# Optimization experiments

Hardware: AMD Instinct MI355X
Metric: run time of the kernel (lower is better)

Reference implementation:

```python
import jax, jax.numpy as jnp
import numpy as np

# Module constants (from init_kwargs)
X_RANGE = (-10.0, 10.0)
Y_RANGE = (-10.0, 10.0)
N_X = 64
N_Y = 64
B = 16
N_CTX = 1024


def make_grid():
    # x counted forward, y counted backwards (image-row convention):
    # grid[k*N_X + j] = (xs[j], ys[k]) with ys from max to min.
    xs = jnp.linspace(X_RANGE[0], X_RANGE[1], N_X, dtype=jnp.float32)
    ys = jnp.linspace(Y_RANGE[1], Y_RANGE[0], N_Y, dtype=jnp.float32)
    gx, gy = jnp.meshgrid(xs, ys)          # each (N_Y, N_X)
    return jnp.stack([gx, gy], axis=-1).reshape(-1, 2)  # (G, 2)


def setup_inputs() -> dict:
    key = jax.random.key(0)
    k1, k2 = jax.random.split(key)
    X = jax.random.uniform(k1, (B, N_CTX, 2), dtype=jnp.float32,
                           minval=X_RANGE[0], maxval=X_RANGE[1])
    Y = jax.random.normal(k2, (B, N_CTX, 2), dtype=jnp.float32)
    log_l_scale = jnp.zeros((), dtype=jnp.float32)  # log(1.0)
    return {"X": X, "Y": Y, "log_l_scale": log_l_scale}


def reference(X, Y, log_l_scale):
    grid = make_grid()                                  # (G, 2)
    l = jnp.exp(log_l_scale)
    # squared distances via expansion to avoid a (B,G,n,2) intermediate
    g2 = jnp.sum(grid * grid, axis=-1)                  # (G,)
    x2 = jnp.sum(X * X, axis=-1)                        # (B, n)
    gx = jnp.einsum('gd,bnd->bgn', grid, X)             # (B, G, n)
    d2 = g2[None, :, None] + x2[:, None, :] - 2.0 * gx  # (B, G, n)
    Gram = jnp.exp(-0.5 * d2 / (l * l))                 # RBF kernel, B=1
    # expand Y with a leading ones (density) channel
    ones = jnp.ones(Y.shape[:2] + (1,), dtype=Y.dtype)
    EY = jnp.concatenate([ones, Y], axis=-1)            # (B, n, 3)
    FM = jnp.einsum('bgn,bnc->bgc', Gram, EY)           # (B, G, 3)
    dens = FM[..., 0:1]
    FM = jnp.concatenate([dens, FM[..., 1:] / dens], axis=-1)
    # (B, G, 3) -> (B, 3, N_Y, N_X)
    return FM.reshape(X.shape[0], N_Y, N_X, 3).transpose(0, 3, 1, 2)
```

## Files before the change

kernel.cpp:

```cpp
#include <hip/hip_runtime.h>
#include <hip/hip_bf16.h>
#include <math.h>


#define NB     16
#define NCTX   1024
#define NG     4096
#define NSPLIT 16
#define NC     64

__global__ __launch_bounds__(256, 1)
void ee_partial(const float* __restrict__ X,
                const float* __restrict__ Y,
                const float* __restrict__ log_l_scale,
                float* __restrict__ ws) {
    const int b  = blockIdx.x >> 4;
    const int nc = blockIdx.x & 15;
    const int n0 = nc * NC;

    const float step  = 20.0f / 63.0f;
    const float scale = -0.72134752044448170f * expf(-2.0f * log_l_scale[0]);

    __shared__ float  wx[NC][64];
    __shared__ float  wy[NC][64];
    __shared__ float2 sy[NC];

    const float2* Xb = (const float2*)(X + (size_t)b * NCTX * 2);
    const float2* Yb = (const float2*)(Y + (size_t)b * NCTX * 2);

    for (int idx = threadIdx.x; idx < NC * 64; idx += 256) {
        const int j = idx >> 6, i = idx & 63;
        const float2 xv = Xb[n0 + j];
        const float dx = (-10.0f + step * (float)i) - xv.x;
        const float dy = ( 10.0f - step * (float)i) - xv.y;
        wx[j][i] = exp2f(dx * dx * scale);
        wy[j][i] = exp2f(dy * dy * scale);
    }
    if (threadIdx.x < NC) sy[threadIdx.x] = Yb[n0 + threadIdx.x];
    __syncthreads();

    const int tx = threadIdx.x & 15;
    const int ty = threadIdx.x >> 4;
    const int ix0 = tx * 4;
    const int iy0 = ty * 4;

    float4 ad[4] = {{0,0,0,0},{0,0,0,0},{0,0,0,0},{0,0,0,0}};
    float4 a1[4] = {{0,0,0,0},{0,0,0,0},{0,0,0,0},{0,0,0,0}};
    float4 a2[4] = {{0,0,0,0},{0,0,0,0},{0,0,0,0},{0,0,0,0}};

#pragma unroll 4
    for (int n = 0; n < NC; ++n) {
        const float4 wxv = *(const float4*)&wx[n][ix0];
        const float4 wyv = *(const float4*)&wy[n][iy0];
        const float2 yv  = sy[n];
        const float wys[4] = {wyv.x, wyv.y, wyv.z, wyv.w};
#pragma unroll
        for (int s = 0; s < 4; ++s) {
            const float w  = wys[s];
            const float q1 = w * yv.x;
            const float q2 = w * yv.y;
            ad[s].x = fmaf(wxv.x, w, ad[s].x);  ad[s].y = fmaf(wxv.y, w, ad[s].y);
            ad[s].z = fmaf(wxv.z, w, ad[s].z);  ad[s].w = fmaf(wxv.w, w, ad[s].w);
            a1[s].x = fmaf(wxv.x, q1, a1[s].x); a1[s].y = fmaf(wxv.y, q1, a1[s].y);
            a1[s].z = fmaf(wxv.z, q1, a1[s].z); a1[s].w = fmaf(wxv.w, q1, a1[s].w);
            a2[s].x = fmaf(wxv.x, q2, a2[s].x); a2[s].y = fmaf(wxv.y, q2, a2[s].y);
            a2[s].z = fmaf(wxv.z, q2, a2[s].z); a2[s].w = fmaf(wxv.w, q2, a2[s].w);
        }
    }

    float* base = ws + ((size_t)(b * NSPLIT + nc)) * 3 * NG;
#pragma unroll
    for (int s = 0; s < 4; ++s) {
        const int g = (iy0 + s) * 64 + ix0;
        *(float4*)&base[g]          = ad[s];
        *(float4*)&base[NG + g]     = a1[s];
        *(float4*)&base[2*NG + g]   = a2[s];
    }
}

__global__ __launch_bounds__(256)
void ee_reduce(const float* __restrict__ ws, float* __restrict__ out) {
    const int t = blockIdx.x * 256 + threadIdx.x;
    const int b = t >> 12, g = t & 4095;
    const float* base = ws + (size_t)b * NSPLIT * 3 * NG;
    float a0 = 0, a1 = 0, a2 = 0;
#pragma unroll
    for (int nc = 0; nc < NSPLIT; ++nc) {
        const float* p = base + nc * 3 * NG;
        a0 += p[g];
        a1 += p[NG + g];
        a2 += p[2 * NG + g];
    }
    const float inv = 1.0f / a0;
    float* ob = out + (size_t)b * 3 * NG;
    ob[g]          = a0;
    ob[NG + g]     = a1 * inv;
    ob[2 * NG + g] = a2 * inv;
}

extern "C" void kernel_launch(void* const* d_in, const int* in_sizes, int n_in,
                              void* d_out, int out_size, void* d_ws, size_t ws_size,
                              hipStream_t stream) {
    const float* X    = (const float*)d_in[0];
    const float* Y    = (const float*)d_in[1];
    const float* logl = (const float*)d_in[2];
    float* out = (float*)d_out;
    float* ws  = (float*)d_ws;

    ee_partial<<<dim3(NB * NSPLIT), dim3(256), 0, stream>>>(X, Y, logl, ws);
    ee_reduce <<<dim3(NB * NG / 256), dim3(256), 0, stream>>>(ws, out);
}
```

Before: 72.62 us.

## Fuse partial and reduce kernels by tiling grid instead of splitting context

```diff
diff --git a/kernel.cpp b/kernel.cpp
--- a/kernel.cpp
+++ b/kernel.cpp
@@ -1,101 +1,91 @@
 #include <hip/hip_runtime.h>
-#include <hip/hip_bf16.h>
 #include <math.h>
 
 
 #define NB     16
 #define NCTX   1024
 #define NG     4096
-#define NSPLIT 16
-#define NC     64
+#define NSTAGE 128
+#define NCHUNK (NCTX / NSTAGE)
+#define ROWLEN (NSTAGE + 4)
 
 __global__ __launch_bounds__(256, 1)
-void ee_partial(const float* __restrict__ X,
-                const float* __restrict__ Y,
-                const float* __restrict__ log_l_scale,
-                float* __restrict__ ws) {
-    const int b  = blockIdx.x >> 4;
-    const int nc = blockIdx.x & 15;
-    const int n0 = nc * NC;
+void ee_fused(const float* __restrict__ X,
+              const float* __restrict__ Y,
+              const float* __restrict__ log_l_scale,
+              float* __restrict__ out) {
+    const int b    = blockIdx.x >> 4;
+    const int tile = blockIdx.x & 15;
+    const int ix0  = (tile & 3) * 16;
+    const int iy0  = (tile >> 2) * 16;
 
     const float step  = 20.0f / 63.0f;
     const float scale = -0.72134752044448170f * expf(-2.0f * log_l_scale[0]);
 
-    __shared__ float  wx[NC][64];
-    __shared__ float  wy[NC][64];
-    __shared__ float2 sy[NC];
+    __shared__ float wxs[2][16][ROWLEN];
+    __shared__ float wys[2][16][ROWLEN];
+    __shared__ float y0s[2][NSTAGE];
+    __shared__ float y1s[2][NSTAGE];
 
     const float2* Xb = (const float2*)(X + (size_t)b * NCTX * 2);
     const float2* Yb = (const float2*)(Y + (size_t)b * NCTX * 2);
 
-    for (int idx = threadIdx.x; idx < NC * 64; idx += 256) {
-        const int j = idx >> 6, i = idx & 63;
-        const float2 xv = Xb[n0 + j];
-        const float dx = (-10.0f + step * (float)i) - xv.x;
-        const float dy = ( 10.0f - step * (float)i) - xv.y;
-        wx[j][i] = exp2f(dx * dx * scale);
-        wy[j][i] = exp2f(dy * dy * scale);
-    }
-    if (threadIdx.x < NC) sy[threadIdx.x] = Yb[n0 + threadIdx.x];
+    const int t   = threadIdx.x;
+    const int ixl = t & 15;
+    const int iyl = t >> 4;
+
+    auto build = [&](int c, int p) {
+        const int n0 = c * NSTAGE;
+        const int n  = t & (NSTAGE - 1);
+        const int ih = t >> 7;
+        const float2 xv = Xb[n0 + n];
+        const float bx = -10.0f + step * (float)ix0 - xv.x;
+        const float by =  10.0f - step * (float)iy0 - xv.y;
+#pragma unroll
+        for (int e = 0; e < 8; ++e) {
+            const int i = 2 * e + ih;
+            const float dx = bx + step * (float)i;
+            const float dy = by - step * (float)i;
+            wxs[p][i][n] = exp2f(dx * dx * scale);
+            wys[p][i][n] = exp2f(dy * dy * scale);
+        }
+        if (t < NSTAGE) {
+            const float2 yv = Yb[n0 + t];
+            y0s[p][t] = yv.x;
+            y1s[p][t] = yv.y;
+        }
+    };
+
+    float dens = 0.0f, s1 = 0.0f, s2 = 0.0f;
+
+    build(0, 0);
     __syncthreads();
 
-    const int tx = threadIdx.x & 15;
-    const int ty = threadIdx.x >> 4;
-    const int ix0 = tx * 4;
-    const int iy0 = ty * 4;
-
-    float4 ad[4] = {{0,0,0,0},{0,0,0,0},{0,0,0,0},{0,0,0,0}};
-    float4 a1[4] = {{0,0,0,0},{0,0,0,0},{0,0,0,0},{0,0,0,0}};
-    float4 a2[4] = {{0,0,0,0},{0,0,0,0},{0,0,0,0},{0,0,0,0}};
+    for (int c = 0; c < NCHUNK; ++c) {
+        const int p = c & 1;
+        if (c + 1 < NCHUNK) build(c + 1, p ^ 1);
 
 #pragma unroll 4
-    for (int n = 0; n < NC; ++n) {
-        const float4 wxv = *(const float4*)&wx[n][ix0];
-        const float4 wyv = *(const float4*)&wy[n][iy0];
-        const float2 yv  = sy[n];
-        const float wys[4] = {wyv.x, wyv.y, wyv.z, wyv.w};
-#pragma unroll
-        for (int s = 0; s < 4; ++s) {
-            const float w  = wys[s];
-            const float q1 = w * yv.x;
-            const float q2 = w * yv.y;
-            ad[s].x = fmaf(wxv.x, w, ad[s].x);  ad[s].y = fmaf(wxv.y, w, ad[s].y);
-            ad[s].z = fmaf(wxv.z, w, ad[s].z);  ad[s].w = fmaf(wxv.w, w, ad[s].w);
-            a1[s].x = fmaf(wxv.x, q1, a1[s].x); a1[s].y = fmaf(wxv.y, q1, a1[s].y);
-            a1[s].z = fmaf(wxv.z, q1, a1[s].z); a1[s].w = fmaf(wxv.w, q1, a1[s].w);
-            a2[s].x = fmaf(wxv.x, q2, a2[s].x); a2[s].y = fmaf(wxv.y, q2, a2[s].y);
-            a2[s].z = fmaf(wxv.z, q2, a2[s].z); a2[s].w = fmaf(wxv.w, q2, a2[s].w);
+        for (int n4 = 0; n4 < NSTAGE; n4 += 4) {
+            const float4 wx4 = *(const float4*)&wxs[p][ixl][n4];
+            const float4 wy4 = *(const float4*)&wys[p][iyl][n4];
+            const float4 ya  = *(const float4*)&y0s[p][n4];
+            const float4 yb  = *(const float4*)&y1s[p][n4];
+            float w;
+            w = wx4.x * wy4.x; dens += w; s1 = fmaf(w, ya.x, s1); s2 = fmaf(w, yb.x, s2);
+            w = wx4.y * wy4.y; dens += w; s1 = fmaf(w, ya.y, s1); s2 = fmaf(w, yb.y, s2);
+            w = wx4.z * wy4.z; dens += w; s1 = fmaf(w, ya.z, s1); s2 = fmaf(w, yb.z, s2);
+            w = wx4.w * wy4.w; dens += w; s1 = fmaf(w, ya.w, s1); s2 = fmaf(w, yb.w, s2);
         }
+        __syncthreads();
     }
 
-    float* base = ws + ((size_t)(b * NSPLIT + nc)) * 3 * NG;
-#pragma unroll
-    for (int s = 0; s < 4; ++s) {
-        const int g = (iy0 + s) * 64 + ix0;
-        *(float4*)&base[g]          = ad[s];
-        *(float4*)&base[NG + g]     = a1[s];
-        *(float4*)&base[2*NG + g]   = a2[s];
-    }
-}
-
-__global__ __launch_bounds__(256)
-void ee_reduce(const float* __restrict__ ws, float* __restrict__ out) {
-    const int t = blockIdx.x * 256 + threadIdx.x;
-    const int b = t >> 12, g = t & 4095;
-    const float* base = ws + (size_t)b * NSPLIT * 3 * NG;
-    float a0 = 0, a1 = 0, a2 = 0;
-#pragma unroll
-    for (int nc = 0; nc < NSPLIT; ++nc) {
-        const float* p = base + nc * 3 * NG;
-        a0 += p[g];
-        a1 += p[NG + g];
-        a2 += p[2 * NG + g];
-    }
-    const float inv = 1.0f / a0;
+    const int g = (iy0 + iyl) * 64 + (ix0 + ixl);
     float* ob = out + (size_t)b * 3 * NG;
-    ob[g]          = a0;
-    ob[NG + g]     = a1 * inv;
-    ob[2 * NG + g] = a2 * inv;
+    const float inv = 1.0f / dens;
+    ob[g]          = dens;
+    ob[NG + g]     = s1 * inv;
+    ob[2 * NG + g] = s2 * inv;
 }
 
 extern "C" void kernel_launch(void* const* d_in, const int* in_sizes, int n_in,
@@ -105,8 +95,7 @@
     const float* Y    = (const float*)d_in[1];
     const float* logl = (const float*)d_in[2];
     float* out = (float*)d_out;
-    float* ws  = (float*)d_ws;
+    (void)d_ws; (void)ws_size;
 
-    ee_partial<<<dim3(NB * NSPLIT), dim3(256), 0, stream>>>(X, Y, logl, ws);
-    ee_reduce <<<dim3(NB * NG / 256), dim3(256), 0, stream>>>(ws, out);
+    ee_fused<<<dim3(NB * 16), dim3(256), 0, stream>>>(X, Y, logl, out);
 }
```

New measurement: 80.46 us. 10.8% more time.
